# Performance work log

Hardware: AMD Instinct MI355X
Metric: run time of the kernel (lower is better)

Reference implementation:

```python
import jax, jax.numpy as jnp
import numpy as np
from jax import lax

B = 32  # CS block size


def _conv(x, w, stride=1, pad=0):
    return lax.conv_general_dilated(
        x, w, window_strides=(stride, stride),
        padding=[(pad, pad), (pad, pad)],
        dimension_numbers=("NCHW", "OIHW", "NCHW"))


def _prelu(x, a):
    return jnp.where(x >= 0, x, a * x)


def _reshape_concat(x):
    # x: [N, B*B, h, w]; channel c = j*B + i maps to block pixel (i, j)
    # (tmp.view(B,B).permute(1,0) in the torch code). Blocks tile rows by
    # dim2 (h) and cols by dim3 (w). Vectorized depth-to-space + transpose.
    N, C, h, w = x.shape
    x5 = x.reshape(N, B, B, h, w)            # dims: (N, j, i, h, w)
    x5 = jnp.transpose(x5, (0, 3, 2, 4, 1))  # (N, h, i, w, j)
    return x5.reshape(N, 1, h * B, w * B)


def setup_inputs() -> dict:
    key = jax.random.key(0)
    ks = jax.random.split(key, 6)
    N, H, W = 16, 256, 256
    csnb = int(0.25 * B * B)  # 256
    inp = {
        "x": jax.random.normal(ks[0], (N, 1, H, W), jnp.float32),
        "W_cs": jax.random.normal(ks[1], (csnb, 1, B, B), jnp.float32) * 0.03,
        "W_init": jax.random.normal(ks[2], (B * B, csnb, 1, 1), jnp.float32) * 0.06,
        "W_first": jax.random.normal(ks[3], (64, 1, 3, 3), jnp.float32) * 0.3,
        "W_blk": jax.random.normal(ks[4], (64, 64, 3, 3), jnp.float32) * 0.04,
        "W_last": jax.random.normal(ks[5], (1, 64, 3, 3), jnp.float32) * 0.04,
        "a_main": jnp.full((1,), 0.1, jnp.float32),
        "a_blk": jnp.full((1,), 0.1, jnp.float32),
    }
    return inp


def reference(x, W_cs, W_init, W_first, W_blk, W_last, a_main, a_blk):
    # CS sampling: [N,1,H,W] -> [N,csnb,H/B,W/B]
    outcsy = _conv(x, W_cs, stride=B, pad=0)
    # initial reconstruction: 1x1 conv to B*B channels
    out = _conv(outcsy, W_init, stride=1, pad=0)
    out_initrec = _reshape_concat(out)          # [N,1,H,W]
    out = _prelu(_conv(out_initrec, W_first, pad=1), a_main)
    # same SORTRes_block (shared weights) applied 4 times
    for _ in range(4):
        o1 = _conv(out, W_blk, pad=1)
        o2 = _prelu(o1, a_blk)
        o3 = _conv(o2, W_blk, pad=1)
        out = _prelu(out + o3, a_blk)
    out = _conv(out + out_initrec, W_last, pad=1)
    return (out, outcsy, out_initrec)
```

## Files before the change

kernel.cpp:

```cpp
#include <hip/hip_runtime.h>
#include <hip/hip_bf16.h>
#include <initializer_list>


#define HW 65536
#define IMG 4194304

typedef __attribute__((ext_vector_type(8))) short short8;
typedef __attribute__((ext_vector_type(4))) float f32x4;

__device__ __forceinline__ float bf2f(unsigned short u) {
    union { unsigned u; float f; } v; v.u = ((unsigned)u) << 16; return v.f;
}
__device__ __forceinline__ unsigned short f2bf(float f) {
    union { float f; unsigned u; } v; v.f = f;
    unsigned r = v.u + 0x7FFF + ((v.u >> 16) & 1);
    return (unsigned short)(r >> 16);
}

__global__ void k_wcsT(const float* __restrict__ Wcs, float* __restrict__ WT)
{
    int e = blockIdx.x * 256 + threadIdx.x;
    int k = e >> 8, c = e & 255;
    WT[(long)k * 256 + c] = Wcs[(long)c * 1024 + k];
}

__global__ void k_winitT(const float* __restrict__ Wi, float* __restrict__ WT)
{
    int e = blockIdx.x * 256 + threadIdx.x;
    int ci = e >> 10, cc = e & 1023;
    WT[e] = Wi[(long)cc * 256 + ci];
}

__global__ __launch_bounds__(256) void k_cs2(const float* __restrict__ x,
        const float* __restrict__ WT, float* __restrict__ outcsy)
{
    __shared__ float xs[2][1024];
    const int b = blockIdx.x;
    const int tid = threadIdx.x;
#pragma unroll
    for (int t = 0; t < 2; ++t) {
        int p = b * 2 + t;
        int wb = p & 7, hb = (p >> 3) & 7, n = p >> 6;
#pragma unroll
        for (int i = 0; i < 4; ++i) {
            int k = tid + 256 * i;
            int ii = k >> 5, jj = k & 31;
            xs[t][k] = x[(long)n * HW + (hb * 32 + ii) * 256 + wb * 32 + jj];
        }
    }
    __syncthreads();
    float a0 = 0.f, a1 = 0.f;
    for (int k = 0; k < 1024; k += 8) {
#pragma unroll
        for (int u = 0; u < 8; ++u) {
            float wv = WT[(long)(k + u) * 256 + tid];
            a0 += wv * xs[0][k + u];
            a1 += wv * xs[1][k + u];
        }
    }
#pragma unroll
    for (int t = 0; t < 2; ++t) {
        int p = b * 2 + t;
        int wb = p & 7, hb = (p >> 3) & 7, n = p >> 6;
        float a = t ? a1 : a0;
        outcsy[(long)n * 16384 + tid * 64 + hb * 8 + wb] = a;
    }
}

__global__ __launch_bounds__(256) void k_init2(const float* __restrict__ outcsy,
        const float* __restrict__ WT, float* __restrict__ initrec)
{
    __shared__ float ys[2][256];
    __shared__ float ov[2][1024];
    const int b = blockIdx.x;
    const int np = b & 7, s = b >> 3;
    const int wb = s & 7, hb = s >> 3;
    const int tid = threadIdx.x;
#pragma unroll
    for (int i = 0; i < 2; ++i) {
        int idx = tid + 256 * i;
        int t = idx >> 8, c = idx & 255;
        ys[t][c] = outcsy[(long)(np * 2 + t) * 16384 + c * 64 + s];
    }
    __syncthreads();
#pragma unroll
    for (int q4 = 0; q4 < 4; ++q4) {
        int cc = q4 * 256 + tid;
        float a0 = 0.f, a1 = 0.f;
        for (int ci = 0; ci < 256; ci += 8) {
#pragma unroll
            for (int u = 0; u < 8; ++u) {
                float wv = WT[(long)(ci + u) * 1024 + cc];
                a0 += wv * ys[0][ci + u];
                a1 += wv * ys[1][ci + u];
            }
        }
        int i = cc & 31, j = cc >> 5;
        ov[0][i * 32 + j] = a0;
        ov[1][i * 32 + j] = a1;
    }
    __syncthreads();
#pragma unroll
    for (int t = 0; t < 2; ++t) {
        int n = np * 2 + t;
#pragma unroll
        for (int i2 = 0; i2 < 4; ++i2) {
            int p = i2 * 256 + tid;
            int i = p >> 5, j = p & 31;
            initrec[(long)n * HW + (hb * 32 + i) * 256 + wb * 32 + j] = ov[t][p];
        }
    }
}

__global__ __launch_bounds__(256) void k_first(const float* __restrict__ initrec,
        const float* __restrict__ Wf, unsigned short* __restrict__ A,
        const float* __restrict__ alpha_p)
{
    const int bid = blockIdx.x;
    const int tx = bid & 15, ty = (bid >> 4) & 15, n = bid >> 8;
    const int tid = threadIdx.x;
    const int x = (tx << 4) + (tid & 15), y = (ty << 4) + (tid >> 4);
    const float* ip = initrec + (long)n * HW;

    float in[9];
#pragma unroll
    for (int ky = 0; ky < 3; ++ky)
#pragma unroll
        for (int kx = 0; kx < 3; ++kx) {
            int iy = y + ky - 1, ix = x + kx - 1;
            in[ky * 3 + kx] = ((unsigned)iy < 256u && (unsigned)ix < 256u)
                                  ? ip[iy * 256 + ix] : 0.f;
        }

    const float alpha = alpha_p[0];
    unsigned short* op = &A[(((long)n * 256 + y) * 256 + x) * 64];
#pragma unroll
    for (int c8 = 0; c8 < 8; ++c8) {
        short8 ov;
#pragma unroll
        for (int j = 0; j < 8; ++j) {
            const float* wp = &Wf[(c8 * 8 + j) * 9];
            float a = 0.f;
#pragma unroll
            for (int t = 0; t < 9; ++t) a += wp[t] * in[t];
            a = a >= 0.f ? a : alpha * a;
            ov[j] = (short)f2bf(a);
        }
        *(short8*)&op[c8 * 8] = ov;
    }
}

__global__ void k_wprep(const float* __restrict__ Wb, unsigned short* __restrict__ Wp)
{
    int e = blockIdx.x * 256 + threadIdx.x;
    int cc = e / 18432, r = e % 18432;
    int tap = r / 2048, r2 = r % 2048;
    int nt = (r2 >> 9) & 3, l = (r2 >> 3) & 63, j = r2 & 7;
    int co = nt * 16 + (l & 15);
    int ci = cc * 32 + (l >> 4) * 8 + j;
    Wp[e] = f2bf(Wb[co * 576 + ci * 9 + tap]);
}

__global__ __launch_bounds__(256, 2) void k_res(const unsigned short* __restrict__ src,
        unsigned short* __restrict__ dst, const unsigned short* __restrict__ Wp,
        const float* __restrict__ alpha_p)
{
    __shared__ short halo[16000];
    __shared__ short o2b[23328];

    const int tid = threadIdx.x;
    const int bid = blockIdx.x;
    const int tx = bid & 15, ty = (bid >> 4) & 15, n = bid >> 8;
    const int x0 = tx * 16, y0 = ty * 16;
    const int w = tid >> 6, lane = tid & 63;
    const int q = lane >> 4, mm = lane & 15;
    const float alpha = alpha_p[0];
    const unsigned short* sb = src + (long)n * IMG;

    int pb1[6];
#pragma unroll
    for (int i = 0; i < 6; ++i) {
        int p = (w + 4 * i) * 16 + mm;
        p = p < 323 ? p : 323;
        pb1[i] = p + 2 * (p / 18);
    }

    short8 bcur[4], bnxt[4];
#pragma unroll
    for (int nt = 0; nt < 4; ++nt)
        bcur[nt] = *(const short8*)&Wp[(size_t)(nt * 512 + lane * 8)];

    const f32x4 zz = {0.f, 0.f, 0.f, 0.f};
    f32x4 acc1[6][4];
#pragma unroll
    for (int i = 0; i < 6; ++i)
#pragma unroll
        for (int nt = 0; nt < 4; ++nt) acc1[i][nt] = zz;

    for (int cc = 0; cc < 2; ++cc) {
        if (cc) __syncthreads();
#pragma unroll
        for (int i = 0; i < 7; ++i) {
            int idx = tid + 256 * i;
            if (idx < 1600) {
                int pix = idx >> 2, part = idx & 3;
                int row = pix / 20, col = pix - row * 20;
                int gy = y0 + row - 2, gx = x0 + col - 2;
                short8 v = {0, 0, 0, 0, 0, 0, 0, 0};
                if ((unsigned)gy < 256u && (unsigned)gx < 256u)
                    v = *(const short8*)&sb[((long)gy * 256 + gx) * 64 + cc * 32 + part * 8];
                *(short8*)&halo[pix * 40 + part * 8] = v;
            }
        }
        __syncthreads();

#pragma unroll
        for (int tap = 0; tap < 9; ++tap) {
            const int s = cc * 9 + tap;
            const int sn = (s + 1) % 18;
            const int ccn = sn / 9, tapn = sn % 9;
#pragma unroll
            for (int nt = 0; nt < 4; ++nt)
                bnxt[nt] = *(const short8*)&Wp[(size_t)ccn * 18432 +
                                               (size_t)((tapn * 4 + nt) * 512 + lane * 8)];
            const int ky = tap / 3, kx = tap % 3;
            const int toff = (ky * 20 + kx) * 40 + q * 8;
#pragma unroll
            for (int i = 0; i < 6; ++i) {
                short8 af = *(const short8*)&halo[pb1[i] * 40 + toff];
#pragma unroll
                for (int nt = 0; nt < 4; ++nt)
                    acc1[i][nt] = __builtin_amdgcn_mfma_f32_16x16x32_bf16(
                        af, bcur[nt], acc1[i][nt], 0, 0, 0);
            }
#pragma unroll
            for (int nt = 0; nt < 4; ++nt) bcur[nt] = bnxt[nt];
        }
    }

#pragma unroll
    for (int i = 0; i < 6; ++i) {
        int t = w + 4 * i;
        if (t < 21) {
#pragma unroll
            for (int r = 0; r < 4; ++r) {
                int p = t * 16 + q * 4 + r;
                p = p < 323 ? p : 323;
                int rho = p / 18, gam = p - 18 * rho;
                bool valid = (unsigned)(y0 - 1 + rho) < 256u &&
                             (unsigned)(x0 - 1 + gam) < 256u;
#pragma unroll
                for (int nt = 0; nt < 4; ++nt) {
                    float v = acc1[i][nt][r];
                    v = v >= 0.f ? v : alpha * v;
                    o2b[p * 72 + nt * 16 + mm] = valid ? (short)f2bf(v) : (short)0;
                }
            }
        }
    }
    __syncthreads();

    f32x4 acc2[4][4];
#pragma unroll
    for (int mt = 0; mt < 4; ++mt)
#pragma unroll
        for (int nt = 0; nt < 4; ++nt) acc2[mt][nt] = zz;

    for (int cc = 0; cc < 2; ++cc) {
#pragma unroll
        for (int tap = 0; tap < 9; ++tap) {
            const int s = cc * 9 + tap;
            const int sn = (s + 1) % 18;
#pragma unroll
            for (int nt = 0; nt < 4; ++nt)
                bnxt[nt] = *(const short8*)&Wp[(size_t)(sn / 9) * 18432 +
                                               (size_t)(((sn % 9) * 4 + nt) * 512 + lane * 8)];
            const int ky = tap / 3, kx = tap % 3;
#pragma unroll
            for (int mt = 0; mt < 4; ++mt) {
                short8 af = *(const short8*)&o2b[((4 * w + mt + ky) * 18 + mm + kx) * 72 +
                                                 cc * 32 + q * 8];
#pragma unroll
                for (int nt = 0; nt < 4; ++nt)
                    acc2[mt][nt] = __builtin_amdgcn_mfma_f32_16x16x32_bf16(
                        af, bcur[nt], acc2[mt][nt], 0, 0, 0);
            }
#pragma unroll
            for (int nt = 0; nt < 4; ++nt) bcur[nt] = bnxt[nt];
        }
    }
    __syncthreads();

    unsigned short* ob = (unsigned short*)o2b;
#pragma unroll
    for (int h = 0; h < 2; ++h) {
        if ((w >> 1) == h) {
#pragma unroll
            for (int mt = 0; mt < 4; ++mt) {
                int row = 4 * w + mt - 8 * h;
#pragma unroll
                for (int nt = 0; nt < 4; ++nt)
#pragma unroll
                    for (int r = 0; r < 4; ++r) {
                        int xx = q * 4 + r;
                        ob[(row * 16 + xx) * 64 + nt * 16 + mm] = f2bf(acc2[mt][nt][r]);
                    }
            }
        }
        __syncthreads();
#pragma unroll
        for (int i = 0; i < 4; ++i) {
            int e = (tid + 256 * i) * 8;
            int co = e & 63, xx = (e >> 6) & 15, row = 8 * h + (e >> 10);
            long g = (((long)n * 256 + y0 + row) * 256 + (x0 + xx)) * 64 + co;
            short8 cv = *(short8*)&ob[e];
            short8 rv = *(const short8*)&src[(long)n * IMG +
                                             ((long)(y0 + row) * 256 + x0 + xx) * 64 + co];
            short8 ov;
#pragma unroll
            for (int j = 0; j < 8; ++j) {
                float v = bf2f((unsigned short)cv[j]) + bf2f((unsigned short)rv[j]);
                v = (v >= 0.f) ? v : alpha * v;
                ov[j] = (short)f2bf(v);
            }
            *(short8*)&dst[(long)n * IMG + ((long)(y0 + row) * 256 + x0 + xx) * 64 + co] = ov;
        }
        __syncthreads();
    }
}

__global__ __launch_bounds__(256) void k_last(const unsigned short* __restrict__ A,
        const float* __restrict__ initrec, const float* __restrict__ Wl,
        float* __restrict__ out0)
{
    __shared__ short ibuf[23328];
    const int bid = blockIdx.x;
    const int tx = bid & 15, ty = (bid >> 4) & 15, n = bid >> 8;
    const int x0 = tx * 16, y0 = ty * 16;
    const int tid = threadIdx.x;
    const unsigned short* Ab = A + (long)n * IMG;

#pragma unroll
    for (int i = 0; i < 11; ++i) {
        int idx = tid + 256 * i;
        if (idx < 2592) {
            int pix = idx >> 3, part = idx & 7;
            int row = pix / 18, col = pix - row * 18;
            int gy = y0 + row - 1, gx = x0 + col - 1;
            short8 v = {0, 0, 0, 0, 0, 0, 0, 0};
            if ((unsigned)gy < 256u && (unsigned)gx < 256u)
                v = *(const short8*)&Ab[((long)gy * 256 + gx) * 64 + part * 8];
            *(short8*)&ibuf[pix * 72 + part * 8] = v;
        }
    }
    __syncthreads();

    float wsum[9];
#pragma unroll
    for (int k = 0; k < 9; ++k) wsum[k] = 0.f;
    for (int ci = 0; ci < 64; ++ci)
#pragma unroll
        for (int k = 0; k < 9; ++k) wsum[k] += Wl[ci * 9 + k];

    const int x = tid & 15, y = tid >> 4;
    const float* ip = initrec + (long)n * HW;
    float acc = 0.f;
#pragma unroll
    for (int ky = 0; ky < 3; ++ky) {
#pragma unroll
        for (int kx = 0; kx < 3; ++kx) {
            const int tap = ky * 3 + kx;
            const short* p = &ibuf[((y + ky) * 18 + (x + kx)) * 72];
#pragma unroll
            for (int c8 = 0; c8 < 8; ++c8) {
                short8 av = *(const short8*)&p[c8 * 8];
#pragma unroll
                for (int j = 0; j < 8; ++j)
                    acc += Wl[(c8 * 8 + j) * 9 + tap] * bf2f((unsigned short)av[j]);
            }
            int gy = y0 + y + ky - 1, gx = x0 + x + kx - 1;
            if ((unsigned)gy < 256u && (unsigned)gx < 256u)
                acc += wsum[tap] * ip[gy * 256 + gx];
        }
    }
    out0[((long)n * 256 + y0 + y) * 256 + (x0 + x)] = acc;
}

extern "C" void kernel_launch(void* const* d_in, const int* in_sizes, int n_in,
                              void* d_out, int out_size, void* d_ws, size_t ws_size,
                              hipStream_t stream)
{
    const float* x     = (const float*)d_in[0];
    const float* Wcs   = (const float*)d_in[1];
    const float* Winit = (const float*)d_in[2];
    const float* Wf    = (const float*)d_in[3];
    const float* Wb    = (const float*)d_in[4];
    const float* Wl    = (const float*)d_in[5];
    const float* amain = (const float*)d_in[6];
    const float* ablk  = (const float*)d_in[7];

    float* out0    = (float*)d_out;
    float* outcsy  = out0 + 1048576;
    float* initrec = outcsy + 262144;

    const size_t EXTRA = 73728 + 2 * 1048576;
    unsigned short* A = (unsigned short*)d_ws;
    int nc = 1;
    for (int c : {16, 8, 4, 2, 1})
        if ((size_t)(16 + c) * IMG * 2 + EXTRA <= ws_size) { nc = c; break; }
    unsigned short* Bt   = A + (size_t)16 * IMG;
    unsigned short* Wp   = Bt + (size_t)nc * IMG;
    float*          WcsT = (float*)(Wp + 36864);
    float*          WinT = WcsT + 262144;

    k_wcsT<<<1024, 256, 0, stream>>>(Wcs, WcsT);
    k_winitT<<<1024, 256, 0, stream>>>(Winit, WinT);
    k_wprep<<<144, 256, 0, stream>>>(Wb, Wp);

    k_cs2<<<512, 256, 0, stream>>>(x, WcsT, outcsy);
    k_init2<<<512, 256, 0, stream>>>(outcsy, WinT, initrec);
    k_first<<<4096, 256, 0, stream>>>(initrec, Wf, A, amain);

    for (int n0 = 0; n0 < 16; n0 += nc) {
        unsigned short* Ac = A + (size_t)n0 * IMG;
        for (int i = 0; i < 4; ++i) {
            const unsigned short* s = (i & 1) ? Bt : Ac;
            unsigned short*       d = (i & 1) ? Ac : Bt;
            k_res<<<nc * 256, 256, 0, stream>>>(s, d, Wp, ablk);
        }
    }
    k_last<<<4096, 256, 0, stream>>>(A, initrec, Wl, out0);
}
```

Measured before the change: 1.125 ms.

## Merge res-block LDS buffers and permute channels to raise occupancy

The residual-block kernel now uses one shared-memory buffer for both the input halo and the intermediate activations instead of two, cutting LDS per block so launch bounds can ask for 3 blocks per CU. To make the intermediate writes vectorized (4 shorts per store), the intermediate channel order is permuted and a second, channel-permuted copy of the weights is prepared for the second convolution. The epilogue is also simplified into a single pass over all 16 rows instead of two halves with extra barriers. The cost is an extra barrier before reusing the buffer, a larger weight buffer, and tighter register limits that could cause spills.

```diff
diff --git a/kernel.cpp b/kernel.cpp
--- a/kernel.cpp
+++ b/kernel.cpp
@@ -7,6 +7,7 @@
 #define IMG 4194304
 
 typedef __attribute__((ext_vector_type(8))) short short8;
+typedef __attribute__((ext_vector_type(4))) short short4v;
 typedef __attribute__((ext_vector_type(4))) float f32x4;
 
 __device__ __forceinline__ float bf2f(unsigned short u) {
@@ -154,20 +155,21 @@
 __global__ void k_wprep(const float* __restrict__ Wb, unsigned short* __restrict__ Wp)
 {
     int e = blockIdx.x * 256 + threadIdx.x;
-    int cc = e / 18432, r = e % 18432;
+    int buf = e / 36864, r0 = e % 36864;
+    int cc = r0 / 18432, r = r0 % 18432;
     int tap = r / 2048, r2 = r % 2048;
     int nt = (r2 >> 9) & 3, l = (r2 >> 3) & 63, j = r2 & 7;
     int co = nt * 16 + (l & 15);
-    int ci = cc * 32 + (l >> 4) * 8 + j;
+    int k = cc * 32 + (l >> 4) * 8 + j;
+    int ci = buf ? ((k & 3) * 16 + (k >> 2)) : k;
     Wp[e] = f2bf(Wb[co * 576 + ci * 9 + tap]);
 }
 
-__global__ __launch_bounds__(256, 2) void k_res(const unsigned short* __restrict__ src,
-        unsigned short* __restrict__ dst, const unsigned short* __restrict__ Wp,
+__global__ __launch_bounds__(256, 3) void k_res(const unsigned short* __restrict__ src,
+        unsigned short* __restrict__ dst, const unsigned short* __restrict__ WpAll,
         const float* __restrict__ alpha_p)
 {
-    __shared__ short halo[16000];
-    __shared__ short o2b[23328];
+    __shared__ short smem[23328];
 
     const int tid = threadIdx.x;
     const int bid = blockIdx.x;
@@ -189,7 +191,7 @@
     short8 bcur[4], bnxt[4];
 #pragma unroll
     for (int nt = 0; nt < 4; ++nt)
-        bcur[nt] = *(const short8*)&Wp[(size_t)(nt * 512 + lane * 8)];
+        bcur[nt] = *(const short8*)&WpAll[(size_t)((nt * 512) + lane * 8)];
 
     const f32x4 zz = {0.f, 0.f, 0.f, 0.f};
     f32x4 acc1[6][4];
@@ -210,25 +212,25 @@
                 short8 v = {0, 0, 0, 0, 0, 0, 0, 0};
                 if ((unsigned)gy < 256u && (unsigned)gx < 256u)
                     v = *(const short8*)&sb[((long)gy * 256 + gx) * 64 + cc * 32 + part * 8];
-                *(short8*)&halo[pix * 40 + part * 8] = v;
+                *(short8*)&smem[pix * 40 + part * 8] = v;
             }
         }
         __syncthreads();
 
 #pragma unroll
         for (int tap = 0; tap < 9; ++tap) {
-            const int s = cc * 9 + tap;
-            const int sn = (s + 1) % 18;
-            const int ccn = sn / 9, tapn = sn % 9;
+            const int un = cc * 9 + tap + 1;
+            const int ub = un / 18, um = un % 18;
 #pragma unroll
             for (int nt = 0; nt < 4; ++nt)
-                bnxt[nt] = *(const short8*)&Wp[(size_t)ccn * 18432 +
-                                               (size_t)((tapn * 4 + nt) * 512 + lane * 8)];
+                bnxt[nt] = *(const short8*)&WpAll[(size_t)ub * 36864 +
+                           (size_t)(um / 9) * 18432 +
+                           (size_t)(((um % 9) * 4 + nt) * 512 + lane * 8)];
             const int ky = tap / 3, kx = tap % 3;
             const int toff = (ky * 20 + kx) * 40 + q * 8;
 #pragma unroll
             for (int i = 0; i < 6; ++i) {
-                short8 af = *(const short8*)&halo[pb1[i] * 40 + toff];
+                short8 af = *(const short8*)&smem[pb1[i] * 40 + toff];
 #pragma unroll
                 for (int nt = 0; nt < 4; ++nt)
                     acc1[i][nt] = __builtin_amdgcn_mfma_f32_16x16x32_bf16(
@@ -238,6 +240,7 @@
             for (int nt = 0; nt < 4; ++nt) bcur[nt] = bnxt[nt];
         }
     }
+    __syncthreads();
 
 #pragma unroll
     for (int i = 0; i < 6; ++i) {
@@ -250,12 +253,14 @@
                 int rho = p / 18, gam = p - 18 * rho;
                 bool valid = (unsigned)(y0 - 1 + rho) < 256u &&
                              (unsigned)(x0 - 1 + gam) < 256u;
+                short4v ov;
 #pragma unroll
                 for (int nt = 0; nt < 4; ++nt) {
                     float v = acc1[i][nt][r];
                     v = v >= 0.f ? v : alpha * v;
-                    o2b[p * 72 + nt * 16 + mm] = valid ? (short)f2bf(v) : (short)0;
+                    ov[nt] = valid ? (short)f2bf(v) : (short)0;
                 }
+                *(short4v*)&smem[p * 72 + mm * 4] = ov;
             }
         }
     }
@@ -270,17 +275,19 @@
     for (int cc = 0; cc < 2; ++cc) {
 #pragma unroll
         for (int tap = 0; tap < 9; ++tap) {
-            const int s = cc * 9 + tap;
-            const int sn = (s + 1) % 18;
+            const int un0 = 18 + cc * 9 + tap + 1;
+            const int un = un0 < 36 ? un0 : 35;
+            const int um = un % 18;
 #pragma unroll
             for (int nt = 0; nt < 4; ++nt)
-                bnxt[nt] = *(const short8*)&Wp[(size_t)(sn / 9) * 18432 +
-                                               (size_t)(((sn % 9) * 4 + nt) * 512 + lane * 8)];
+                bnxt[nt] = *(const short8*)&WpAll[(size_t)36864 +
+                           (size_t)(um / 9) * 18432 +
+                           (size_t)(((um % 9) * 4 + nt) * 512 + lane * 8)];
             const int ky = tap / 3, kx = tap % 3;
 #pragma unroll
             for (int mt = 0; mt < 4; ++mt) {
-                short8 af = *(const short8*)&o2b[((4 * w + mt + ky) * 18 + mm + kx) * 72 +
-                                                 cc * 32 + q * 8];
+                short8 af = *(const short8*)&smem[((4 * w + mt + ky) * 18 + mm + kx) * 72 +
+                                                  cc * 32 + q * 8];
 #pragma unroll
                 for (int nt = 0; nt < 4; ++nt)
                     acc2[mt][nt] = __builtin_amdgcn_mfma_f32_16x16x32_bf16(
@@ -292,41 +299,35 @@
     }
     __syncthreads();
 
-    unsigned short* ob = (unsigned short*)o2b;
-#pragma unroll
-    for (int h = 0; h < 2; ++h) {
-        if ((w >> 1) == h) {
-#pragma unroll
-            for (int mt = 0; mt < 4; ++mt) {
-                int row = 4 * w + mt - 8 * h;
-#pragma unroll
-                for (int nt = 0; nt < 4; ++nt)
-#pragma unroll
-                    for (int r = 0; r < 4; ++r) {
-                        int xx = q * 4 + r;
-                        ob[(row * 16 + xx) * 64 + nt * 16 + mm] = f2bf(acc2[mt][nt][r]);
-                    }
-            }
-        }
-        __syncthreads();
-#pragma unroll
-        for (int i = 0; i < 4; ++i) {
-            int e = (tid + 256 * i) * 8;
-            int co = e & 63, xx = (e >> 6) & 15, row = 8 * h + (e >> 10);
-            long g = (((long)n * 256 + y0 + row) * 256 + (x0 + xx)) * 64 + co;
-            short8 cv = *(short8*)&ob[e];
-            short8 rv = *(const short8*)&src[(long)n * IMG +
-                                             ((long)(y0 + row) * 256 + x0 + xx) * 64 + co];
-            short8 ov;
-#pragma unroll
-            for (int j = 0; j < 8; ++j) {
-                float v = bf2f((unsigned short)cv[j]) + bf2f((unsigned short)rv[j]);
-                v = (v >= 0.f) ? v : alpha * v;
-                ov[j] = (short)f2bf(v);
-            }
-            *(short8*)&dst[(long)n * IMG + ((long)(y0 + row) * 256 + x0 + xx) * 64 + co] = ov;
-        }
-        __syncthreads();
+    unsigned short* ob = (unsigned short*)smem;
+#pragma unroll
+    for (int mt = 0; mt < 4; ++mt) {
+        int row = 4 * w + mt;
+#pragma unroll
+        for (int nt = 0; nt < 4; ++nt)
+#pragma unroll
+            for (int r = 0; r < 4; ++r) {
+                int xx = q * 4 + r;
+                ob[(row * 16 + xx) * 64 + nt * 16 + mm] = f2bf(acc2[mt][nt][r]);
+            }
+    }
+    __syncthreads();
+#pragma unroll
+    for (int i = 0; i < 8; ++i) {
+        int e = (tid + 256 * i) * 8;
+        int co = e & 63, xx = (e >> 6) & 15, row = e >> 10;
+        long g = (((long)n * 256 + y0 + row) * 256 + (x0 + xx)) * 64 + co;
+        short8 cv = *(short8*)&ob[e];
+        short8 rv = *(const short8*)&src[(long)n * IMG +
+                                         ((long)(y0 + row) * 256 + x0 + xx) * 64 + co];
+        short8 ov;
+#pragma unroll
+        for (int j = 0; j < 8; ++j) {
+            float v = bf2f((unsigned short)cv[j]) + bf2f((unsigned short)rv[j]);
+            v = (v >= 0.f) ? v : alpha * v;
+            ov[j] = (short)f2bf(v);
+        }
+        *(short8*)&dst[(long)n * IMG + ((long)(y0 + row) * 256 + x0 + xx) * 64 + co] = ov;
     }
 }
 
@@ -404,19 +405,19 @@
     float* outcsy  = out0 + 1048576;
     float* initrec = outcsy + 262144;
 
-    const size_t EXTRA = 73728 + 2 * 1048576;
+    const size_t EXTRA = 147456 + 2 * 1048576;
     unsigned short* A = (unsigned short*)d_ws;
     int nc = 1;
     for (int c : {16, 8, 4, 2, 1})
         if ((size_t)(16 + c) * IMG * 2 + EXTRA <= ws_size) { nc = c; break; }
     unsigned short* Bt   = A + (size_t)16 * IMG;
     unsigned short* Wp   = Bt + (size_t)nc * IMG;
-    float*          WcsT = (float*)(Wp + 36864);
+    float*          WcsT = (float*)(Wp + 73728);
     float*          WinT = WcsT + 262144;
 
     k_wcsT<<<1024, 256, 0, stream>>>(Wcs, WcsT);
     k_winitT<<<1024, 256, 0, stream>>>(Winit, WinT);
-    k_wprep<<<144, 256, 0, stream>>>(Wb, Wp);
+    k_wprep<<<288, 256, 0, stream>>>(Wb, Wp);
 
     k_cs2<<<512, 256, 0, stream>>>(x, WcsT, outcsy);
     k_init2<<<512, 256, 0, stream>>>(outcsy, WinT, initrec);
```

Result: slower. 1.302 ms (+15.8%).

## Load full 64-channel halo once into a unified shared buffer in residual kernel

Applied to the files above, without the earlier changes.

The residual-block kernel now loads all 64 input channels of the 20x20 halo in a single pass into one shared buffer. Previously it loaded two 32-channel halves separately with extra barriers. The halo, the intermediate activation and the output staging all alias this buffer, padded to a 76-element pixel stride. The first conv skips the mostly-padded sixth M tile on all waves but wave 0, and the output store is done in one pass rather than two halves. This cuts barriers and wasted MFMAs, but shared-memory use per block changes, which affects occupancy and bank-conflict patterns.

```diff
diff --git a/kernel.cpp b/kernel.cpp
--- a/kernel.cpp
+++ b/kernel.cpp
@@ -166,8 +166,7 @@
         unsigned short* __restrict__ dst, const unsigned short* __restrict__ Wp,
         const float* __restrict__ alpha_p)
 {
-    __shared__ short halo[16000];
-    __shared__ short o2b[23328];
+    __shared__ short smem[30400];
 
     const int tid = threadIdx.x;
     const int bid = blockIdx.x;
@@ -186,6 +185,20 @@
         pb1[i] = p + 2 * (p / 18);
     }
 
+#pragma unroll
+    for (int i = 0; i < 13; ++i) {
+        int idx = tid + 256 * i;
+        if (idx < 3200) {
+            int pix = idx >> 3, part = idx & 7;
+            int row = pix / 20, col = pix - row * 20;
+            int gy = y0 + row - 2, gx = x0 + col - 2;
+            short8 v = {0, 0, 0, 0, 0, 0, 0, 0};
+            if ((unsigned)gy < 256u && (unsigned)gx < 256u)
+                v = *(const short8*)&sb[((long)gy * 256 + gx) * 64 + part * 8];
+            *(short8*)&smem[pix * 76 + part * 8] = v;
+        }
+    }
+
     short8 bcur[4], bnxt[4];
 #pragma unroll
     for (int nt = 0; nt < 4; ++nt)
@@ -198,46 +211,37 @@
 #pragma unroll
         for (int nt = 0; nt < 4; ++nt) acc1[i][nt] = zz;
 
-    for (int cc = 0; cc < 2; ++cc) {
-        if (cc) __syncthreads();
-#pragma unroll
-        for (int i = 0; i < 7; ++i) {
-            int idx = tid + 256 * i;
-            if (idx < 1600) {
-                int pix = idx >> 2, part = idx & 3;
-                int row = pix / 20, col = pix - row * 20;
-                int gy = y0 + row - 2, gx = x0 + col - 2;
-                short8 v = {0, 0, 0, 0, 0, 0, 0, 0};
-                if ((unsigned)gy < 256u && (unsigned)gx < 256u)
-                    v = *(const short8*)&sb[((long)gy * 256 + gx) * 64 + cc * 32 + part * 8];
-                *(short8*)&halo[pix * 40 + part * 8] = v;
-            }
-        }
-        __syncthreads();
-
-#pragma unroll
-        for (int tap = 0; tap < 9; ++tap) {
-            const int s = cc * 9 + tap;
-            const int sn = (s + 1) % 18;
-            const int ccn = sn / 9, tapn = sn % 9;
+    __syncthreads();
+
+#pragma unroll
+    for (int s = 0; s < 18; ++s) {
+        const int cc = s / 9, tap = s % 9;
+        int un = s + 1; un = un < 18 ? un : 0;
+#pragma unroll
+        for (int nt = 0; nt < 4; ++nt)
+            bnxt[nt] = *(const short8*)&Wp[(size_t)(un / 9) * 18432 +
+                       (size_t)(((un % 9) * 4 + nt) * 512 + lane * 8)];
+        const int ky = tap / 3, kx = tap % 3;
+        const int toff = (ky * 20 + kx) * 76 + cc * 32 + q * 8;
+#pragma unroll
+        for (int i = 0; i < 5; ++i) {
+            short8 af = *(const short8*)&smem[pb1[i] * 76 + toff];
 #pragma unroll
             for (int nt = 0; nt < 4; ++nt)
-                bnxt[nt] = *(const short8*)&Wp[(size_t)ccn * 18432 +
-                                               (size_t)((tapn * 4 + nt) * 512 + lane * 8)];
-            const int ky = tap / 3, kx = tap % 3;
-            const int toff = (ky * 20 + kx) * 40 + q * 8;
-#pragma unroll
-            for (int i = 0; i < 6; ++i) {
-                short8 af = *(const short8*)&halo[pb1[i] * 40 + toff];
-#pragma unroll
-                for (int nt = 0; nt < 4; ++nt)
-                    acc1[i][nt] = __builtin_amdgcn_mfma_f32_16x16x32_bf16(
-                        af, bcur[nt], acc1[i][nt], 0, 0, 0);
-            }
-#pragma unroll
-            for (int nt = 0; nt < 4; ++nt) bcur[nt] = bnxt[nt];
-        }
-    }
+                acc1[i][nt] = __builtin_amdgcn_mfma_f32_16x16x32_bf16(
+                    af, bcur[nt], acc1[i][nt], 0, 0, 0);
+        }
+        if (w == 0) {
+            short8 af = *(const short8*)&smem[pb1[5] * 76 + toff];
+#pragma unroll
+            for (int nt = 0; nt < 4; ++nt)
+                acc1[5][nt] = __builtin_amdgcn_mfma_f32_16x16x32_bf16(
+                    af, bcur[nt], acc1[5][nt], 0, 0, 0);
+        }
+#pragma unroll
+        for (int nt = 0; nt < 4; ++nt) bcur[nt] = bnxt[nt];
+    }
+    __syncthreads();
 
 #pragma unroll
     for (int i = 0; i < 6; ++i) {
@@ -254,7 +258,7 @@
                 for (int nt = 0; nt < 4; ++nt) {
                     float v = acc1[i][nt][r];
                     v = v >= 0.f ? v : alpha * v;
-                    o2b[p * 72 + nt * 16 + mm] = valid ? (short)f2bf(v) : (short)0;
+                    smem[p * 76 + nt * 16 + mm] = valid ? (short)f2bf(v) : (short)0;
                 }
             }
         }
@@ -267,66 +271,58 @@
 #pragma unroll
         for (int nt = 0; nt < 4; ++nt) acc2[mt][nt] = zz;
 
-    for (int cc = 0; cc < 2; ++cc) {
-#pragma unroll
-        for (int tap = 0; tap < 9; ++tap) {
-            const int s = cc * 9 + tap;
-            const int sn = (s + 1) % 18;
+#pragma unroll
+    for (int s = 0; s < 18; ++s) {
+        const int cc = s / 9, tap = s % 9;
+        int un = s + 1; un = un < 18 ? un : 17;
+#pragma unroll
+        for (int nt = 0; nt < 4; ++nt)
+            bnxt[nt] = *(const short8*)&Wp[(size_t)(un / 9) * 18432 +
+                       (size_t)(((un % 9) * 4 + nt) * 512 + lane * 8)];
+        const int ky = tap / 3, kx = tap % 3;
+#pragma unroll
+        for (int mt = 0; mt < 4; ++mt) {
+            int pix = (4 * w + mt + ky) * 18 + mm + kx;
+            short8 af = *(const short8*)&smem[pix * 76 + cc * 32 + q * 8];
 #pragma unroll
             for (int nt = 0; nt < 4; ++nt)
-                bnxt[nt] = *(const short8*)&Wp[(size_t)(sn / 9) * 18432 +
-                                               (size_t)(((sn % 9) * 4 + nt) * 512 + lane * 8)];
-            const int ky = tap / 3, kx = tap % 3;
-#pragma unroll
-            for (int mt = 0; mt < 4; ++mt) {
-                short8 af = *(const short8*)&o2b[((4 * w + mt + ky) * 18 + mm + kx) * 72 +
-                                                 cc * 32 + q * 8];
-#pragma unroll
-                for (int nt = 0; nt < 4; ++nt)
-                    acc2[mt][nt] = __builtin_amdgcn_mfma_f32_16x16x32_bf16(
-                        af, bcur[nt], acc2[mt][nt], 0, 0, 0);
+                acc2[mt][nt] = __builtin_amdgcn_mfma_f32_16x16x32_bf16(
+                    af, bcur[nt], acc2[mt][nt], 0, 0, 0);
+        }
+#pragma unroll
+        for (int nt = 0; nt < 4; ++nt) bcur[nt] = bnxt[nt];
+    }
+    __syncthreads();
+
+    unsigned short* ob = (unsigned short*)smem;
+#pragma unroll
+    for (int mt = 0; mt < 4; ++mt) {
+        int row = 4 * w + mt;
+#pragma unroll
+        for (int nt = 0; nt < 4; ++nt)
+#pragma unroll
+            for (int r = 0; r < 4; ++r) {
+                int xx = q * 4 + r;
+                ob[(row * 16 + xx) * 64 + nt * 16 + mm] = f2bf(acc2[mt][nt][r]);
             }
-#pragma unroll
-            for (int nt = 0; nt < 4; ++nt) bcur[nt] = bnxt[nt];
-        }
-    }
-    __syncthreads();
-
-    unsigned short* ob = (unsigned short*)o2b;
-#pragma unroll
-    for (int h = 0; h < 2; ++h) {
-        if ((w >> 1) == h) {
-#pragma unroll
-            for (int mt = 0; mt < 4; ++mt) {
-                int row = 4 * w + mt - 8 * h;
-#pragma unroll
-                for (int nt = 0; nt < 4; ++nt)
-#pragma unroll
-                    for (int r = 0; r < 4; ++r) {
-                        int xx = q * 4 + r;
-                        ob[(row * 16 + xx) * 64 + nt * 16 + mm] = f2bf(acc2[mt][nt][r]);
-                    }
-            }
-        }
-        __syncthreads();
-#pragma unroll
-        for (int i = 0; i < 4; ++i) {
-            int e = (tid + 256 * i) * 8;
-            int co = e & 63, xx = (e >> 6) & 15, row = 8 * h + (e >> 10);
-            long g = (((long)n * 256 + y0 + row) * 256 + (x0 + xx)) * 64 + co;
-            short8 cv = *(short8*)&ob[e];
-            short8 rv = *(const short8*)&src[(long)n * IMG +
-                                             ((long)(y0 + row) * 256 + x0 + xx) * 64 + co];
-            short8 ov;
-#pragma unroll
-            for (int j = 0; j < 8; ++j) {
-                float v = bf2f((unsigned short)cv[j]) + bf2f((unsigned short)rv[j]);
-                v = (v >= 0.f) ? v : alpha * v;
-                ov[j] = (short)f2bf(v);
-            }
-            *(short8*)&dst[(long)n * IMG + ((long)(y0 + row) * 256 + x0 + xx) * 64 + co] = ov;
-        }
-        __syncthreads();
+    }
+    __syncthreads();
+#pragma unroll
+    for (int i = 0; i < 8; ++i) {
+        int e = (tid + 256 * i) * 8;
+        int co = e & 63, xx = (e >> 6) & 15, row = e >> 10;
+        long g = (((long)n * 256 + y0 + row) * 256 + (x0 + xx)) * 64 + co;
+        short8 cv = *(short8*)&ob[e];
+        short8 rv = *(const short8*)&src[(long)n * IMG +
+                                         ((long)(y0 + row) * 256 + x0 + xx) * 64 + co];
+        short8 ov;
+#pragma unroll
+        for (int j = 0; j < 8; ++j) {
+            float v = bf2f((unsigned short)cv[j]) + bf2f((unsigned short)rv[j]);
+            v = (v >= 0.f) ? v : alpha * v;
+            ov[j] = (short)f2bf(v);
+        }
+        *(short8*)&dst[(long)n * IMG + ((long)(y0 + row) * 256 + x0 + xx) * 64 + co] = ov;
     }
 }
 
```

Result: no change. 1.141 ms (+1.5%).
